# Performance work log

Hardware: AMD Instinct MI355X
Metric: run time of the kernel (lower is better)

The kernel has to match this reference:

```python
import jax, jax.numpy as jnp
import numpy as np

B, C, K, T = 8, 256, 64, 1000
NORM_EPS = 1e-12


def setup_inputs() -> dict:
    key = jax.random.key(0)
    k_x, k_codes, k_scales = jax.random.split(key, 3)
    init_val = 1.0 / (K * C) ** 0.5
    x = jax.random.normal(k_x, (B, C, T), dtype=jnp.float32)
    codes = jax.random.uniform(k_codes, (C, K), dtype=jnp.float32,
                               minval=-init_val, maxval=init_val)
    scales = jax.random.uniform(k_scales, (K,), dtype=jnp.float32,
                                minval=0.0, maxval=1.0)
    return {"x": x, "codes": codes, "scales": scales}


def l2_normalize(t, axis, eps=NORM_EPS):
    n = jnp.sqrt(jnp.sum(t * t, axis=axis, keepdims=True))
    n = jnp.maximum(n, eps)
    return t / n


def reference(x, codes, scales):
    # x: (B, C, T); codes: (C, K); scales: (K,)
    residual = x[:, :, None, :] - codes[None, :, :, None]      # (B, C, K, T)
    residual_l2sqr = jnp.sum(residual * residual, axis=1)      # (B, K, T)
    weights_tc = jax.nn.softmax(-scales[None, :, None] * residual_l2sqr, axis=1)  # softmax over codes K
    embeddings = jnp.einsum('bckt,bkt->bkc', residual, weights_tc) / x.shape[-1]  # (B, K, C)
    embeddings = l2_normalize(embeddings, axis=-1)
    return embeddings
```

## Files before the change

### kernel.cpp

```cpp
#include <hip/hip_runtime.h>
#include <stdint.h>

constexpr int Bn  = 8;
constexpr int Cn  = 256;
constexpr int Kn  = 64;
constexpr int Tn  = 1000;
constexpr int CH  = 16;
constexpr int NCH = 64;
constexpr int TW  = 256;
constexpr int NTQ = 4;

constexpr int XT_P = 264;
constexpr int MW_P = 20;
constexpr int XC_P = 264;

typedef float f32x4 __attribute__((ext_vector_type(4)));
typedef __bf16 bf16x8 __attribute__((ext_vector_type(8)));

__device__ __forceinline__ unsigned short f2bf(float f) {
    unsigned u = __float_as_uint(f);
    return (unsigned short)((u + 0x7FFFu + ((u >> 16) & 1u)) >> 16);
}

union BF8 { unsigned short u[8]; bf16x8 v; };

__global__ __launch_bounds__(256) void lde_w(
    const float* __restrict__ x,
    const float* __restrict__ codes,
    const float* __restrict__ scales,
    unsigned short* __restrict__ w_g,
    float* __restrict__ Sp)
{
    __shared__ __align__(16) unsigned short xT[CH * XT_P];
    __shared__ float Mw[Kn * MW_P];
    __shared__ float xsqp[64 * 17];
    __shared__ float xsq[CH];
    __shared__ float csqs[Kn];
    __shared__ float spw[4 * 64];

    const int tid  = threadIdx.x;
    const int wave = tid >> 6;
    const int lane = tid & 63;
    const int n    = lane & 15;
    const int q    = lane >> 4;
    const int b    = blockIdx.x >> 6;
    const int ch   = blockIdx.x & 63;
    const int t0   = ch * CH;
    const float* xb = x + (size_t)b * Cn * Tn;

    {
        const int tf = tid & 3;
        float sq0 = 0.f, sq1 = 0.f, sq2 = 0.f, sq3 = 0.f;
#pragma unroll
        for (int r = 0; r < 4; ++r) {
            int c = (tid >> 2) + 64 * r;
            int t = t0 + 4 * tf;
            float4 v;
            if (t + 3 < Tn) {
                v = *(const float4*)(xb + c * Tn + t);
            } else {
                v.x = (t     < Tn) ? xb[c * Tn + t]     : 0.f;
                v.y = (t + 1 < Tn) ? xb[c * Tn + t + 1] : 0.f;
                v.z = (t + 2 < Tn) ? xb[c * Tn + t + 2] : 0.f;
                v.w = (t + 3 < Tn) ? xb[c * Tn + t + 3] : 0.f;
            }
            xT[(4 * tf + 0) * XT_P + c] = f2bf(v.x);
            xT[(4 * tf + 1) * XT_P + c] = f2bf(v.y);
            xT[(4 * tf + 2) * XT_P + c] = f2bf(v.z);
            xT[(4 * tf + 3) * XT_P + c] = f2bf(v.w);
            sq0 = fmaf(v.x, v.x, sq0);
            sq1 = fmaf(v.y, v.y, sq1);
            sq2 = fmaf(v.z, v.z, sq2);
            sq3 = fmaf(v.w, v.w, sq3);
        }
        float* xp = xsqp + (tid >> 2) * 17 + 4 * tf;
        xp[0] = sq0; xp[1] = sq1; xp[2] = sq2; xp[3] = sq3;
    }
    __syncthreads();

    if (tid < CH) {
        float a = 0.f;
#pragma unroll
        for (int i = 0; i < 64; ++i) a += xsqp[i * 17 + tid];
        xsq[tid] = a;
    }

    {
        const int kglob = wave * 16 + n;
        const float* cod = codes + (q * 8) * Kn + kglob;
        float csq_part = 0.f;
        f32x4 acc = {0.f, 0.f, 0.f, 0.f};
#pragma unroll
        for (int c0 = 0; c0 < Cn; c0 += 32) {
            float cf[8];
#pragma unroll
            for (int j = 0; j < 8; ++j) cf[j] = cod[(size_t)(c0 + j) * Kn];
            BF8 aF;
#pragma unroll
            for (int j = 0; j < 8; ++j) {
                csq_part = fmaf(cf[j], cf[j], csq_part);
                aF.u[j] = f2bf(cf[j]);
            }
            bf16x8 bF = *(const bf16x8*)(xT + n * XT_P + c0 + q * 8);
            acc = __builtin_amdgcn_mfma_f32_16x16x32_bf16(aF.v, bF, acc, 0, 0, 0);
        }
        csq_part += __shfl_xor(csq_part, 16, 64);
        csq_part += __shfl_xor(csq_part, 32, 64);
        if (q == 0) csqs[kglob] = csq_part;
#pragma unroll
        for (int r = 0; r < 4; ++r)
            Mw[(wave * 16 + q * 4 + r) * MW_P + n] = acc[r];
    }
    __syncthreads();

    {
        const float sc = scales[lane];
        const float cq = csqs[lane];
        unsigned short wh[4];
        float sp = 0.f;
#pragma unroll
        for (int j = 0; j < 4; ++j) {
            int t = wave * 4 + j;
            float m     = Mw[lane * MW_P + t];
            float logit = -sc * (xsq[t] - 2.f * m + cq);
            float mx = logit;
#pragma unroll
            for (int off = 32; off >= 1; off >>= 1)
                mx = fmaxf(mx, __shfl_xor(mx, off, 64));
            float e = __expf(logit - mx);
            float s = e;
#pragma unroll
            for (int off = 32; off >= 1; off >>= 1)
                s += __shfl_xor(s, off, 64);
            float wv = e / s;
            if (t0 + t >= Tn) wv = 0.f;
            sp += wv;
            wh[j] = f2bf(wv);
        }
        *(ushort4*)(w_g + ((size_t)(b * NCH + ch) * Kn + lane) * CH + wave * 4) =
            make_ushort4(wh[0], wh[1], wh[2], wh[3]);
        spw[wave * 64 + lane] = sp;
    }
    __syncthreads();
    if (wave == 0) {
        float s4 = spw[lane] + spw[64 + lane] + spw[128 + lane] + spw[192 + lane];
        Sp[((size_t)b * Kn + lane) * NCH + ch] = s4;
    }
}

__global__ __launch_bounds__(256) void lde_pool(
    const float* __restrict__ x,
    const unsigned short* __restrict__ w_g,
    float* __restrict__ part)
{
    __shared__ __align__(16) unsigned short xc[16 * XC_P];

    const int tid  = threadIdx.x;
    const int wave = tid >> 6;
    const int lane = tid & 63;
    const int n    = lane & 15;
    const int q    = lane >> 4;
    const int bid  = blockIdx.x;
    const int b    = bid >> 6;
    const int ct   = (bid >> 2) & 15;
    const int tq   = bid & 3;
    const int c0   = ct * 16;
    const int tw0  = tq * TW;
    const float* xb = x + (size_t)(b * Cn + c0) * Tn;

#pragma unroll
    for (int r = 0; r < 4; ++r) {
        int idx = r * 256 + tid;
        int cl = idx >> 6, tf = idx & 63;
        int t = tw0 + 4 * tf;
        float4 v;
        if (t + 3 < Tn) {
            v = *(const float4*)(xb + cl * Tn + t);
        } else {
            v.x = (t     < Tn) ? xb[cl * Tn + t]     : 0.f;
            v.y = (t + 1 < Tn) ? xb[cl * Tn + t + 1] : 0.f;
            v.z = (t + 2 < Tn) ? xb[cl * Tn + t + 2] : 0.f;
            v.w = (t + 3 < Tn) ? xb[cl * Tn + t + 3] : 0.f;
        }
        *(ushort4*)(xc + cl * XC_P + 4 * tf) =
            make_ushort4(f2bf(v.x), f2bf(v.y), f2bf(v.z), f2bf(v.w));
    }
    __syncthreads();

    f32x4 acc = {0.f, 0.f, 0.f, 0.f};
#pragma unroll
    for (int s = 0; s < 8; ++s) {
        int tg  = tw0 + s * 32 + q * 8;
        int chh = tg >> 4;
        int tl  = tg & 15;
        bf16x8 aF = *(const bf16x8*)(w_g + ((size_t)(b * NCH + chh) * Kn + wave * 16 + n) * CH + tl);
        bf16x8 bF = *(const bf16x8*)(xc + n * XC_P + s * 32 + q * 8);
        acc = __builtin_amdgcn_mfma_f32_16x16x32_bf16(aF, bF, acc, 0, 0, 0);
    }
    float* pb = part + ((size_t)(b * NTQ + tq) * Kn + wave * 16 + q * 4) * Cn + c0 + n;
#pragma unroll
    for (int r = 0; r < 4; ++r)
        pb[(size_t)r * Cn] = acc[r];
}

__global__ __launch_bounds__(256) void lde_fin(
    const float* __restrict__ part,
    const float* __restrict__ Sp,
    const float* __restrict__ codes,
    float* __restrict__ out)
{
    const int b    = blockIdx.x >> 6;
    const int k    = blockIdx.x & 63;
    const int tid  = threadIdx.x;
    const int lane = tid & 63;
    const int wave = tid >> 6;

    __shared__ float red[4];
    __shared__ float Ss;

    if (wave == 0) {
        float s = Sp[((size_t)b * Kn + k) * NCH + lane];
#pragma unroll
        for (int off = 32; off >= 1; off >>= 1) s += __shfl_xor(s, off, 64);
        if (lane == 0) Ss = s;
    }
    __syncthreads();
    const float S = Ss;

    const int c = tid;
    const float* pb = part + (size_t)b * NTQ * Kn * Cn + k * Cn + c;
    float val = pb[0] + pb[(size_t)Kn * Cn] + pb[(size_t)2 * Kn * Cn] + pb[(size_t)3 * Kn * Cn];

    float e = (val - codes[c * Kn + k] * S) * (1.0f / (float)Tn);

    float qq = e * e;
#pragma unroll
    for (int off = 32; off >= 1; off >>= 1) qq += __shfl_xor(qq, off, 64);
    if (lane == 0) red[wave] = qq;
    __syncthreads();
    float nn = sqrtf(red[0] + red[1] + red[2] + red[3]);

    out[((size_t)b * Kn + k) * Cn + c] = e / fmaxf(nn, 1e-12f);
}

extern "C" void kernel_launch(void* const* d_in, const int* in_sizes, int n_in,
                              void* d_out, int out_size, void* d_ws, size_t ws_size,
                              hipStream_t stream) {
    const float* x      = (const float*)d_in[0];
    const float* codes  = (const float*)d_in[1];
    const float* scales = (const float*)d_in[2];
    float* out = (float*)d_out;

    char* ws = (char*)d_ws;
    float*          part = (float*)ws;
    unsigned short* w_g  = (unsigned short*)(ws + (2u << 20));
    float*          Sp   = (float*)(ws + (3u << 20));

    lde_w   <<<Bn * NCH,      256, 0, stream>>>(x, codes, scales, w_g, Sp);
    lde_pool<<<Bn * 16 * NTQ, 256, 0, stream>>>(x, w_g, part);
    lde_fin <<<Bn * Kn,       256, 0, stream>>>(part, Sp, codes, out);
}
```

Before: 75.20 us.

## Fuse softmax-weight and pooling kernels into one per-time-chunk kernel

Merges the weight kernel and the pooling kernel into a single 512-thread kernel over 32-step time chunks. Each block keeps bf16 x in shared memory in both orientations and computes its partial K×C embedding directly, so the bf16 weights no longer go through global memory and x is read once instead of twice. The cost is a much larger partial buffer (32 chunks × K × C per batch, about 16 MB), which the finalize kernel must now reduce over 32 slices instead of 4, plus higher shared-memory use per block.

```diff
diff --git a/kernel.cpp b/kernel.cpp
--- a/kernel.cpp
+++ b/kernel.cpp
@@ -5,14 +5,13 @@
 constexpr int Cn  = 256;
 constexpr int Kn  = 64;
 constexpr int Tn  = 1000;
-constexpr int CH  = 16;
-constexpr int NCH = 64;
-constexpr int TW  = 256;
-constexpr int NTQ = 4;
+constexpr int CH  = 32;
+constexpr int NCH = 32;
 
 constexpr int XT_P = 264;
-constexpr int MW_P = 20;
-constexpr int XC_P = 264;
+constexpr int XC_P = 40;
+constexpr int MW_P = 33;
+constexpr int WL_P = 40;
 
 typedef float f32x4 __attribute__((ext_vector_type(4)));
 typedef __bf16 bf16x8 __attribute__((ext_vector_type(8)));
@@ -24,70 +23,79 @@
 
 union BF8 { unsigned short u[8]; bf16x8 v; };
 
-__global__ __launch_bounds__(256) void lde_w(
+__global__ __launch_bounds__(512, 2) void lde_wp(
     const float* __restrict__ x,
     const float* __restrict__ codes,
     const float* __restrict__ scales,
-    unsigned short* __restrict__ w_g,
+    float* __restrict__ part,
     float* __restrict__ Sp)
 {
     __shared__ __align__(16) unsigned short xT[CH * XT_P];
+    __shared__ __align__(16) unsigned short xc[Cn * XC_P];
+    __shared__ __align__(16) unsigned short wl[Kn * WL_P];
     __shared__ float Mw[Kn * MW_P];
-    __shared__ float xsqp[64 * 17];
+    __shared__ float xsqp[64 * 33];
     __shared__ float xsq[CH];
     __shared__ float csqs[Kn];
-    __shared__ float spw[4 * 64];
+    __shared__ float spw[8 * 64];
 
     const int tid  = threadIdx.x;
     const int wave = tid >> 6;
     const int lane = tid & 63;
     const int n    = lane & 15;
     const int q    = lane >> 4;
-    const int b    = blockIdx.x >> 6;
-    const int ch   = blockIdx.x & 63;
+    const int b    = blockIdx.x >> 5;
+    const int ch   = blockIdx.x & 31;
     const int t0   = ch * CH;
-    const float* xb = x + (size_t)b * Cn * Tn;
-
-    {
-        const int tf = tid & 3;
-        float sq0 = 0.f, sq1 = 0.f, sq2 = 0.f, sq3 = 0.f;
+    const float sc = scales[lane];
+
+    {
+        const int tf = tid & 7;
+        const int cg = tid >> 3;
+        const float* xb = x + (size_t)b * Cn * Tn;
+        float s0 = 0.f, s1 = 0.f, s2 = 0.f, s3 = 0.f;
+        const int t = t0 + 4 * tf;
 #pragma unroll
         for (int r = 0; r < 4; ++r) {
-            int c = (tid >> 2) + 64 * r;
-            int t = t0 + 4 * tf;
+            int c = cg + 64 * r;
             float4 v;
             if (t + 3 < Tn) {
-                v = *(const float4*)(xb + c * Tn + t);
+                v = *(const float4*)(xb + (size_t)c * Tn + t);
             } else {
-                v.x = (t     < Tn) ? xb[c * Tn + t]     : 0.f;
-                v.y = (t + 1 < Tn) ? xb[c * Tn + t + 1] : 0.f;
-                v.z = (t + 2 < Tn) ? xb[c * Tn + t + 2] : 0.f;
-                v.w = (t + 3 < Tn) ? xb[c * Tn + t + 3] : 0.f;
+                v.x = (t     < Tn) ? xb[(size_t)c * Tn + t]     : 0.f;
+                v.y = (t + 1 < Tn) ? xb[(size_t)c * Tn + t + 1] : 0.f;
+                v.z = (t + 2 < Tn) ? xb[(size_t)c * Tn + t + 2] : 0.f;
+                v.w = (t + 3 < Tn) ? xb[(size_t)c * Tn + t + 3] : 0.f;
             }
-            xT[(4 * tf + 0) * XT_P + c] = f2bf(v.x);
-            xT[(4 * tf + 1) * XT_P + c] = f2bf(v.y);
-            xT[(4 * tf + 2) * XT_P + c] = f2bf(v.z);
-            xT[(4 * tf + 3) * XT_P + c] = f2bf(v.w);
-            sq0 = fmaf(v.x, v.x, sq0);
-            sq1 = fmaf(v.y, v.y, sq1);
-            sq2 = fmaf(v.z, v.z, sq2);
-            sq3 = fmaf(v.w, v.w, sq3);
-        }
-        float* xp = xsqp + (tid >> 2) * 17 + 4 * tf;
-        xp[0] = sq0; xp[1] = sq1; xp[2] = sq2; xp[3] = sq3;
-    }
-    __syncthreads();
-
-    if (tid < CH) {
+            unsigned short h0 = f2bf(v.x), h1 = f2bf(v.y);
+            unsigned short h2 = f2bf(v.z), h3 = f2bf(v.w);
+            xT[(4 * tf + 0) * XT_P + c] = h0;
+            xT[(4 * tf + 1) * XT_P + c] = h1;
+            xT[(4 * tf + 2) * XT_P + c] = h2;
+            xT[(4 * tf + 3) * XT_P + c] = h3;
+            *(ushort4*)(xc + c * XC_P + 4 * tf) = make_ushort4(h0, h1, h2, h3);
+            s0 = fmaf(v.x, v.x, s0);
+            s1 = fmaf(v.y, v.y, s1);
+            s2 = fmaf(v.z, v.z, s2);
+            s3 = fmaf(v.w, v.w, s3);
+        }
+        float* xp = xsqp + cg * 33 + 4 * tf;
+        xp[0] = s0; xp[1] = s1; xp[2] = s2; xp[3] = s3;
+    }
+    __syncthreads();
+
+    if (tid < 32) {
         float a = 0.f;
 #pragma unroll
-        for (int i = 0; i < 64; ++i) a += xsqp[i * 17 + tid];
+        for (int g = 0; g < 64; ++g) a += xsqp[g * 33 + tid];
         xsq[tid] = a;
     }
 
     {
-        const int kglob = wave * 16 + n;
-        const float* cod = codes + (q * 8) * Kn + kglob;
+        const int kt    = wave >> 1;
+        const int tt    = wave & 1;
+        const int kglob = kt * 16 + n;
+        const float* cod = codes + (size_t)(q * 8) * Kn + kglob;
         float csq_part = 0.f;
         f32x4 acc = {0.f, 0.f, 0.f, 0.f};
 #pragma unroll
@@ -101,26 +109,24 @@
                 csq_part = fmaf(cf[j], cf[j], csq_part);
                 aF.u[j] = f2bf(cf[j]);
             }
-            bf16x8 bF = *(const bf16x8*)(xT + n * XT_P + c0 + q * 8);
+            bf16x8 bF = *(const bf16x8*)(xT + (tt * 16 + n) * XT_P + c0 + q * 8);
             acc = __builtin_amdgcn_mfma_f32_16x16x32_bf16(aF.v, bF, acc, 0, 0, 0);
         }
         csq_part += __shfl_xor(csq_part, 16, 64);
         csq_part += __shfl_xor(csq_part, 32, 64);
-        if (q == 0) csqs[kglob] = csq_part;
+        if (tt == 0 && q == 0) csqs[kglob] = csq_part;
 #pragma unroll
         for (int r = 0; r < 4; ++r)
-            Mw[(wave * 16 + q * 4 + r) * MW_P + n] = acc[r];
-    }
-    __syncthreads();
-
-    {
-        const float sc = scales[lane];
+            Mw[(kt * 16 + q * 4 + r) * MW_P + tt * 16 + n] = acc[r];
+    }
+    __syncthreads();
+
+    {
         const float cq = csqs[lane];
-        unsigned short wh[4];
         float sp = 0.f;
 #pragma unroll
         for (int j = 0; j < 4; ++j) {
-            int t = wave * 4 + j;
+            int t = 4 * wave + j;
             float m     = Mw[lane * MW_P + t];
             float logit = -sc * (xsq[t] - 2.f * m + cq);
             float mx = logit;
@@ -135,72 +141,35 @@
             float wv = e / s;
             if (t0 + t >= Tn) wv = 0.f;
             sp += wv;
-            wh[j] = f2bf(wv);
-        }
-        *(ushort4*)(w_g + ((size_t)(b * NCH + ch) * Kn + lane) * CH + wave * 4) =
-            make_ushort4(wh[0], wh[1], wh[2], wh[3]);
+            wl[lane * WL_P + t] = f2bf(wv);
+        }
         spw[wave * 64 + lane] = sp;
     }
     __syncthreads();
-    if (wave == 0) {
-        float s4 = spw[lane] + spw[64 + lane] + spw[128 + lane] + spw[192 + lane];
-        Sp[((size_t)b * Kn + lane) * NCH + ch] = s4;
-    }
-}
-
-__global__ __launch_bounds__(256) void lde_pool(
-    const float* __restrict__ x,
-    const unsigned short* __restrict__ w_g,
-    float* __restrict__ part)
-{
-    __shared__ __align__(16) unsigned short xc[16 * XC_P];
-
-    const int tid  = threadIdx.x;
-    const int wave = tid >> 6;
-    const int lane = tid & 63;
-    const int n    = lane & 15;
-    const int q    = lane >> 4;
-    const int bid  = blockIdx.x;
-    const int b    = bid >> 6;
-    const int ct   = (bid >> 2) & 15;
-    const int tq   = bid & 3;
-    const int c0   = ct * 16;
-    const int tw0  = tq * TW;
-    const float* xb = x + (size_t)(b * Cn + c0) * Tn;
-
-#pragma unroll
-    for (int r = 0; r < 4; ++r) {
-        int idx = r * 256 + tid;
-        int cl = idx >> 6, tf = idx & 63;
-        int t = tw0 + 4 * tf;
-        float4 v;
-        if (t + 3 < Tn) {
-            v = *(const float4*)(xb + cl * Tn + t);
-        } else {
-            v.x = (t     < Tn) ? xb[cl * Tn + t]     : 0.f;
-            v.y = (t + 1 < Tn) ? xb[cl * Tn + t + 1] : 0.f;
-            v.z = (t + 2 < Tn) ? xb[cl * Tn + t + 2] : 0.f;
-            v.w = (t + 3 < Tn) ? xb[cl * Tn + t + 3] : 0.f;
-        }
-        *(ushort4*)(xc + cl * XC_P + 4 * tf) =
-            make_ushort4(f2bf(v.x), f2bf(v.y), f2bf(v.z), f2bf(v.w));
-    }
-    __syncthreads();
-
-    f32x4 acc = {0.f, 0.f, 0.f, 0.f};
-#pragma unroll
-    for (int s = 0; s < 8; ++s) {
-        int tg  = tw0 + s * 32 + q * 8;
-        int chh = tg >> 4;
-        int tl  = tg & 15;
-        bf16x8 aF = *(const bf16x8*)(w_g + ((size_t)(b * NCH + chh) * Kn + wave * 16 + n) * CH + tl);
-        bf16x8 bF = *(const bf16x8*)(xc + n * XC_P + s * 32 + q * 8);
-        acc = __builtin_amdgcn_mfma_f32_16x16x32_bf16(aF, bF, acc, 0, 0, 0);
-    }
-    float* pb = part + ((size_t)(b * NTQ + tq) * Kn + wave * 16 + q * 4) * Cn + c0 + n;
-#pragma unroll
-    for (int r = 0; r < 4; ++r)
-        pb[(size_t)r * Cn] = acc[r];
+
+    if (tid < 64) {
+        float s = 0.f;
+#pragma unroll
+        for (int w = 0; w < 8; ++w) s += spw[w * 64 + tid];
+        Sp[((size_t)b * Kn + tid) * NCH + ch] = s;
+    }
+
+    {
+        const int kt    = wave >> 1;
+        const int chalf = (wave & 1) * 128;
+        bf16x8 aF = *(const bf16x8*)(wl + (kt * 16 + n) * WL_P + q * 8);
+        float* pb0 = part + ((size_t)(b * NCH + ch) * Kn + kt * 16 + q * 4) * Cn;
+#pragma unroll
+        for (int s = 0; s < 8; ++s) {
+            int cc = chalf + s * 16;
+            bf16x8 bF = *(const bf16x8*)(xc + (cc + n) * XC_P + q * 8);
+            f32x4 acc = {0.f, 0.f, 0.f, 0.f};
+            acc = __builtin_amdgcn_mfma_f32_16x16x32_bf16(aF, bF, acc, 0, 0, 0);
+#pragma unroll
+            for (int r = 0; r < 4; ++r)
+                pb0[(size_t)r * Cn + cc + n] = acc[r];
+        }
+    }
 }
 
 __global__ __launch_bounds__(256) void lde_fin(
@@ -219,7 +188,7 @@
     __shared__ float Ss;
 
     if (wave == 0) {
-        float s = Sp[((size_t)b * Kn + k) * NCH + lane];
+        float s = (lane < NCH) ? Sp[((size_t)b * Kn + k) * NCH + lane] : 0.f;
 #pragma unroll
         for (int off = 32; off >= 1; off >>= 1) s += __shfl_xor(s, off, 64);
         if (lane == 0) Ss = s;
@@ -228,8 +197,10 @@
     const float S = Ss;
 
     const int c = tid;
-    const float* pb = part + (size_t)b * NTQ * Kn * Cn + k * Cn + c;
-    float val = pb[0] + pb[(size_t)Kn * Cn] + pb[(size_t)2 * Kn * Cn] + pb[(size_t)3 * Kn * Cn];
+    const float* pb = part + (size_t)b * NCH * Kn * Cn + (size_t)k * Cn + c;
+    float val = 0.f;
+#pragma unroll
+    for (int chn = 0; chn < NCH; ++chn) val += pb[(size_t)chn * Kn * Cn];
 
     float e = (val - codes[c * Kn + k] * S) * (1.0f / (float)Tn);
 
@@ -252,11 +223,9 @@
     float* out = (float*)d_out;
 
     char* ws = (char*)d_ws;
-    float*          part = (float*)ws;
-    unsigned short* w_g  = (unsigned short*)(ws + (2u << 20));
-    float*          Sp   = (float*)(ws + (3u << 20));
-
-    lde_w   <<<Bn * NCH,      256, 0, stream>>>(x, codes, scales, w_g, Sp);
-    lde_pool<<<Bn * 16 * NTQ, 256, 0, stream>>>(x, w_g, part);
-    lde_fin <<<Bn * Kn,       256, 0, stream>>>(part, Sp, codes, out);
-}
+    float* part = (float*)ws;
+    float* Sp   = (float*)(ws + (16u << 20));
+
+    lde_wp <<<Bn * NCH, 512, 0, stream>>>(x, codes, scales, part, Sp);
+    lde_fin<<<Bn * Kn,  256, 0, stream>>>(part, Sp, codes, out);
+}
```

Result: no change. 76.39 us (+1.6%).
